# Kernel tuning notes

Measured on AMD Instinct MI355X. Metric: run time of the kernel, lower is better.

Reference implementation:

```python
import jax, jax.numpy as jnp
import numpy as np

N_ITER = 3
EPS = 1e-8


def _squash(v):
    # v: [B, 1, D]; norm over last (feature) dim
    norm = jnp.linalg.norm(v, axis=2, keepdims=True)
    scale = norm ** 2 / (1 + norm ** 2) / (norm + EPS)
    return scale * v


def setup_inputs() -> dict:
    key = jax.random.key(0)
    k1, k2 = jax.random.split(key)
    B, N, D = 64, 4096, 256
    x = jax.random.normal(k1, (B, N, D), dtype=jnp.float32)
    m = jax.random.uniform(k2, (B, N, 1), dtype=jnp.float32)
    return {"x": x, "m": m}


def reference(x, m):
    # x: [B, N, D], m: [B, N, 1]
    x = m * x
    B, N, _ = x.shape
    b = jnp.zeros((B, N, 1), dtype=x.dtype)
    s = None
    for _ in range(N_ITER):
        w = jax.nn.softmax(m * b, axis=1)            # [B, N, 1]
        sigma = jnp.sum(w * x, axis=1, keepdims=True)  # [B, 1, D]  (== bmm(w^T, x))
        s = _squash(sigma)                            # [B, 1, D]
        b_new = jnp.sum(s * x, axis=2, keepdims=True)  # [B, N, 1]
        b = b + b_new
    w = jax.nn.softmax(b, axis=1)                     # [B, N, 1]
    s = s.reshape(s.shape[0], s.shape[-1])            # [B, D]
    w = w.reshape(w.shape[0], w.shape[1])             # [B, N]
    return (w, s)
```

## Files before the change

kernel.cpp:

```cpp
#include <hip/hip_runtime.h>
#include <math.h>

#define BB 64
#define NN 4096
#define DD 256

template<bool FINAL>
__global__ __launch_bounds__(256) void fpass_kernel(
    const float* __restrict__ x, const float* __restrict__ m,
    const float* __restrict__ s_buf, float* __restrict__ b_buf,
    float* __restrict__ part_sig, float* __restrict__ part_M,
    float* __restrict__ part_Z, int P, int rowsPerWave)
{
    const int lane = threadIdx.x & 63;
    const int wib  = threadIdx.x >> 6;
    const int bpb  = P >> 2;
    const int batch = blockIdx.x / bpb;
    const int p = (blockIdx.x % bpb) * 4 + wib;
    const int n0 = p * rowsPerWave;

    const float4 s4 = reinterpret_cast<const float4*>(s_buf + batch * DD)[lane];
    const float4* __restrict__ xr =
        reinterpret_cast<const float4*>(x + ((size_t)batch * NN + n0) * DD) + lane;
    const float* __restrict__ mrow = m + (size_t)batch * NN + n0;
    float* __restrict__ brow = b_buf + (size_t)batch * NN + n0;

    float M = -INFINITY, Z = 0.f;
    float sx = 0.f, sy = 0.f, sz = 0.f, sw = 0.f;

    #pragma unroll 4
    for (int r = 0; r < rowsPerWave; ++r) {
        float4 xv = xr[(size_t)r * (DD / 4)];
        float mn = mrow[r];
        float dp = xv.x * s4.x + xv.y * s4.y + xv.z * s4.z + xv.w * s4.w;
        #pragma unroll
        for (int off = 32; off; off >>= 1) dp += __shfl_xor(dp, off, 64);
        float bn = brow[r] + mn * dp;
        if (lane == 0) brow[r] = bn;
        float l = FINAL ? bn : mn * bn;
        if (l > M) {
            float c = __expf(M - l);
            Z *= c;
            if (!FINAL) { sx *= c; sy *= c; sz *= c; sw *= c; }
            M = l;
        }
        float e = __expf(l - M);
        Z += e;
        if (!FINAL) {
            float wgt = e * mn;
            sx += wgt * xv.x; sy += wgt * xv.y; sz += wgt * xv.z; sw += wgt * xv.w;
        }
    }
    if (!FINAL) {
        reinterpret_cast<float4*>(part_sig + ((size_t)batch * P + p) * DD)[lane] =
            make_float4(sx, sy, sz, sw);
    }
    if (lane == 0) {
        part_M[batch * P + p] = M;
        part_Z[batch * P + p] = Z;
    }
}

template<bool FINAL>
__global__ __launch_bounds__(256) void reduce_kernel(
    const float* __restrict__ part_sig, const float* __restrict__ part_M,
    const float* __restrict__ part_Z, float* __restrict__ s_buf,
    float* __restrict__ s_out, float* __restrict__ MZf, int P)
{
    const int b = blockIdx.x;
    const int t = threadIdx.x;
    __shared__ float red[256];
    __shared__ float csh[128];

    float Mv = (t < P) ? part_M[b * P + t] : -INFINITY;
    red[t] = Mv;
    __syncthreads();
    for (int s = 128; s > 0; s >>= 1) {
        if (t < s) red[t] = fmaxf(red[t], red[t + s]);
        __syncthreads();
    }
    float Mg = red[0];
    __syncthreads();

    float zc = 0.f;
    if (t < P) {
        float c = expf(Mv - Mg);
        csh[t] = c;
        zc = part_Z[b * P + t] * c;
    }
    red[t] = zc;
    __syncthreads();
    for (int s = 128; s > 0; s >>= 1) {
        if (t < s) red[t] += red[t + s];
        __syncthreads();
    }
    float Zg = red[0];

    if (FINAL) {
        if (t == 0) { MZf[2 * b] = Mg; MZf[2 * b + 1] = Zg; }
        return;
    }
    __syncthreads();

    float sig = 0.f;
    for (int p = 0; p < P; ++p)
        sig += csh[p] * part_sig[((size_t)b * P + p) * DD + t];
    sig /= Zg;

    red[t] = sig * sig;
    __syncthreads();
    for (int s = 128; s > 0; s >>= 1) {
        if (t < s) red[t] += red[t + s];
        __syncthreads();
    }
    float n2 = red[0];
    float nrm = sqrtf(n2);
    float scale = n2 / (1.f + n2) / (nrm + 1e-8f);
    float sv = scale * sig;
    s_buf[b * DD + t] = sv;
    if (s_out) s_out[b * DD + t] = sv;
}

__global__ __launch_bounds__(256) void w_kernel(
    const float* __restrict__ b_buf, const float* __restrict__ MZf,
    float* __restrict__ w_out)
{
    int i = blockIdx.x * 256 + threadIdx.x;
    int b = i >> 12;
    w_out[i] = __expf(b_buf[i] - MZf[2 * b]) / MZf[2 * b + 1];
}

extern "C" void kernel_launch(void* const* d_in, const int* in_sizes, int n_in,
                              void* d_out, int out_size, void* d_ws, size_t ws_size,
                              hipStream_t stream)
{
    const float* x = (const float*)d_in[0];
    const float* m = (const float*)d_in[1];
    float* out = (float*)d_out;

    int P = 128;
    auto needBytes = [](int Pv) -> size_t {
        return (size_t)(BB * NN + BB * DD + (size_t)BB * Pv * DD + BB * Pv * 2 + 2 * BB)
               * sizeof(float);
    };
    while (P > 8 && needBytes(P) > ws_size) P >>= 1;

    float* ws       = (float*)d_ws;
    float* b_buf    = ws;
    float* s_buf    = b_buf + BB * NN;
    float* part_sig = s_buf + BB * DD;
    float* part_M   = part_sig + (size_t)BB * P * DD;
    float* part_Z   = part_M + BB * P;
    float* MZf      = part_Z + BB * P;

    hipMemsetAsync(ws, 0, (size_t)(BB * NN + BB * DD) * sizeof(float), stream);

    const int rpw = NN / P;
    const int blocksF = BB * P / 4;
    float* s_final = out + BB * NN;

    for (int it = 0; it < 3; ++it) {
        fpass_kernel<false><<<blocksF, 256, 0, stream>>>(
            x, m, s_buf, b_buf, part_sig, part_M, part_Z, P, rpw);
        reduce_kernel<false><<<BB, 256, 0, stream>>>(
            part_sig, part_M, part_Z, s_buf, (it == 2) ? s_final : nullptr, MZf, P);
    }
    fpass_kernel<true><<<blocksF, 256, 0, stream>>>(
        x, m, s_buf, b_buf, part_sig, part_M, part_Z, P, rpw);
    reduce_kernel<true><<<BB, 256, 0, stream>>>(
        part_sig, part_M, part_Z, s_buf, nullptr, MZf, P);
    w_kernel<<<BB * NN / 256, 256, 0, stream>>>(b_buf, MZf, out);
}
```

Baseline: 512.6 us.

## Unroll fpass rows by four, widen reduce kernel, vectorize softmax writer

The row loop in the fused pass now handles four rows per iteration, batching the x loads, shuffle reductions and the b/m accesses as float4, and uses a branchless online-softmax update. The partial reduction kernel moves to 1024 threads, using wave shuffles for max and sum and splitting the partial-sigma accumulation across four thread groups. The final weight kernel processes float4 per thread with a precomputed reciprocal. These aim to cut memory latency stalls and the serial reduction, at the cost of always computing two exponentials per row and requiring rowsPerWave to be a multiple of four.

```diff
diff --git a/kernel.cpp b/kernel.cpp
--- a/kernel.cpp
+++ b/kernel.cpp
@@ -28,28 +28,51 @@
     float M = -INFINITY, Z = 0.f;
     float sx = 0.f, sy = 0.f, sz = 0.f, sw = 0.f;
 
-    #pragma unroll 4
-    for (int r = 0; r < rowsPerWave; ++r) {
-        float4 xv = xr[(size_t)r * (DD / 4)];
-        float mn = mrow[r];
-        float dp = xv.x * s4.x + xv.y * s4.y + xv.z * s4.z + xv.w * s4.w;
-        #pragma unroll
-        for (int off = 32; off; off >>= 1) dp += __shfl_xor(dp, off, 64);
-        float bn = brow[r] + mn * dp;
-        if (lane == 0) brow[r] = bn;
+    auto upd = [&](float bn, float mn, const float4& xv) {
         float l = FINAL ? bn : mn * bn;
-        if (l > M) {
-            float c = __expf(M - l);
-            Z *= c;
-            if (!FINAL) { sx *= c; sy *= c; sz *= c; sw *= c; }
-            M = l;
-        }
-        float e = __expf(l - M);
-        Z += e;
+        float newM = fmaxf(M, l);
+        float c = __expf(M - newM);
+        float e = __expf(l - newM);
+        Z = Z * c + e;
         if (!FINAL) {
             float wgt = e * mn;
-            sx += wgt * xv.x; sy += wgt * xv.y; sz += wgt * xv.z; sw += wgt * xv.w;
+            sx = sx * c + wgt * xv.x;
+            sy = sy * c + wgt * xv.y;
+            sz = sz * c + wgt * xv.z;
+            sw = sw * c + wgt * xv.w;
         }
+        M = newM;
+    };
+
+    for (int r0 = 0; r0 < rowsPerWave; r0 += 4) {
+        float4 xv0 = xr[(size_t)(r0 + 0) * (DD / 4)];
+        float4 xv1 = xr[(size_t)(r0 + 1) * (DD / 4)];
+        float4 xv2 = xr[(size_t)(r0 + 2) * (DD / 4)];
+        float4 xv3 = xr[(size_t)(r0 + 3) * (DD / 4)];
+        const float4 m4 = *reinterpret_cast<const float4*>(mrow + r0);
+        const float4 b4 = *reinterpret_cast<const float4*>(brow + r0);
+
+        float dp0 = xv0.x * s4.x + xv0.y * s4.y + xv0.z * s4.z + xv0.w * s4.w;
+        float dp1 = xv1.x * s4.x + xv1.y * s4.y + xv1.z * s4.z + xv1.w * s4.w;
+        float dp2 = xv2.x * s4.x + xv2.y * s4.y + xv2.z * s4.z + xv2.w * s4.w;
+        float dp3 = xv3.x * s4.x + xv3.y * s4.y + xv3.z * s4.z + xv3.w * s4.w;
+        #pragma unroll
+        for (int off = 32; off; off >>= 1) {
+            dp0 += __shfl_xor(dp0, off, 64);
+            dp1 += __shfl_xor(dp1, off, 64);
+            dp2 += __shfl_xor(dp2, off, 64);
+            dp3 += __shfl_xor(dp3, off, 64);
+        }
+        float bn0 = b4.x + m4.x * dp0;
+        float bn1 = b4.y + m4.y * dp1;
+        float bn2 = b4.z + m4.z * dp2;
+        float bn3 = b4.w + m4.w * dp3;
+        if (lane == 0)
+            *reinterpret_cast<float4*>(brow + r0) = make_float4(bn0, bn1, bn2, bn3);
+        upd(bn0, m4.x, xv0);
+        upd(bn1, m4.y, xv1);
+        upd(bn2, m4.z, xv2);
+        upd(bn3, m4.w, xv3);
     }
     if (!FINAL) {
         reinterpret_cast<float4*>(part_sig + ((size_t)batch * P + p) * DD)[lane] =
@@ -62,63 +85,67 @@
 }
 
 template<bool FINAL>
-__global__ __launch_bounds__(256) void reduce_kernel(
+__global__ __launch_bounds__(1024) void reduce_kernel(
     const float* __restrict__ part_sig, const float* __restrict__ part_M,
     const float* __restrict__ part_Z, float* __restrict__ s_buf,
     float* __restrict__ s_out, float* __restrict__ MZf, int P)
 {
     const int b = blockIdx.x;
-    const int t = threadIdx.x;
-    __shared__ float red[256];
+    const int tid = threadIdx.x;
+    __shared__ float red[1024];
     __shared__ float csh[128];
-
-    float Mv = (t < P) ? part_M[b * P + t] : -INFINITY;
-    red[t] = Mv;
+    __shared__ float mg_sh, zg_sh;
+
+    if (tid < 64) {
+        float M0 = (tid < P) ? part_M[b * P + tid] : -INFINITY;
+        float M1 = (tid + 64 < P) ? part_M[b * P + tid + 64] : -INFINITY;
+        float Mm = fmaxf(M0, M1);
+        #pragma unroll
+        for (int off = 32; off; off >>= 1) Mm = fmaxf(Mm, __shfl_xor(Mm, off, 64));
+        float c0 = (tid < P) ? expf(M0 - Mm) : 0.f;
+        float c1 = (tid + 64 < P) ? expf(M1 - Mm) : 0.f;
+        if (tid < P) csh[tid] = c0;
+        if (tid + 64 < P) csh[tid + 64] = c1;
+        float Zs = ((tid < P) ? part_Z[b * P + tid] : 0.f) * c0
+                 + ((tid + 64 < P) ? part_Z[b * P + tid + 64] : 0.f) * c1;
+        #pragma unroll
+        for (int off = 32; off; off >>= 1) Zs += __shfl_xor(Zs, off, 64);
+        if (tid == 0) { mg_sh = Mm; zg_sh = Zs; }
+    }
+    __syncthreads();
+
+    if (FINAL) {
+        if (tid == 0) { MZf[2 * b] = mg_sh; MZf[2 * b + 1] = zg_sh; }
+        return;
+    }
+
+    const int q = tid >> 8;
+    const int d = tid & 255;
+    float sig = 0.f;
+    #pragma unroll 4
+    for (int k = q; k < P; k += 4)
+        sig += csh[k] * part_sig[((size_t)b * P + k) * DD + d];
+    red[tid] = sig;
+    __syncthreads();
+
+    if (tid < 256) {
+        sig = red[tid] + red[tid + 256] + red[tid + 512] + red[tid + 768];
+        sig /= zg_sh;
+        red[tid] = sig * sig;
+    }
     __syncthreads();
     for (int s = 128; s > 0; s >>= 1) {
-        if (t < s) red[t] = fmaxf(red[t], red[t + s]);
+        if (tid < s) red[tid] += red[tid + s];
         __syncthreads();
     }
-    float Mg = red[0];
-    __syncthreads();
-
-    float zc = 0.f;
-    if (t < P) {
-        float c = expf(Mv - Mg);
-        csh[t] = c;
-        zc = part_Z[b * P + t] * c;
-    }
-    red[t] = zc;
-    __syncthreads();
-    for (int s = 128; s > 0; s >>= 1) {
-        if (t < s) red[t] += red[t + s];
-        __syncthreads();
-    }
-    float Zg = red[0];
-
-    if (FINAL) {
-        if (t == 0) { MZf[2 * b] = Mg; MZf[2 * b + 1] = Zg; }
-        return;
-    }
-    __syncthreads();
-
-    float sig = 0.f;
-    for (int p = 0; p < P; ++p)
-        sig += csh[p] * part_sig[((size_t)b * P + p) * DD + t];
-    sig /= Zg;
-
-    red[t] = sig * sig;
-    __syncthreads();
-    for (int s = 128; s > 0; s >>= 1) {
-        if (t < s) red[t] += red[t + s];
-        __syncthreads();
-    }
-    float n2 = red[0];
-    float nrm = sqrtf(n2);
-    float scale = n2 / (1.f + n2) / (nrm + 1e-8f);
-    float sv = scale * sig;
-    s_buf[b * DD + t] = sv;
-    if (s_out) s_out[b * DD + t] = sv;
+    if (tid < 256) {
+        float n2 = red[0];
+        float nrm = sqrtf(n2);
+        float scale = n2 / (1.f + n2) / (nrm + 1e-8f);
+        float sv = scale * sig;
+        s_buf[b * DD + tid] = sv;
+        if (s_out) s_out[b * DD + tid] = sv;
+    }
 }
 
 __global__ __launch_bounds__(256) void w_kernel(
@@ -126,8 +153,16 @@
     float* __restrict__ w_out)
 {
     int i = blockIdx.x * 256 + threadIdx.x;
-    int b = i >> 12;
-    w_out[i] = __expf(b_buf[i] - MZf[2 * b]) / MZf[2 * b + 1];
+    int b = i >> 10;
+    float Mg = MZf[2 * b];
+    float iZ = 1.f / MZf[2 * b + 1];
+    float4 bv = reinterpret_cast<const float4*>(b_buf)[i];
+    float4 wv;
+    wv.x = __expf(bv.x - Mg) * iZ;
+    wv.y = __expf(bv.y - Mg) * iZ;
+    wv.z = __expf(bv.z - Mg) * iZ;
+    wv.w = __expf(bv.w - Mg) * iZ;
+    reinterpret_cast<float4*>(w_out)[i] = wv;
 }
 
 extern "C" void kernel_launch(void* const* d_in, const int* in_sizes, int n_in,
@@ -162,12 +197,12 @@
     for (int it = 0; it < 3; ++it) {
         fpass_kernel<false><<<blocksF, 256, 0, stream>>>(
             x, m, s_buf, b_buf, part_sig, part_M, part_Z, P, rpw);
-        reduce_kernel<false><<<BB, 256, 0, stream>>>(
+        reduce_kernel<false><<<BB, 1024, 0, stream>>>(
             part_sig, part_M, part_Z, s_buf, (it == 2) ? s_final : nullptr, MZf, P);
     }
     fpass_kernel<true><<<blocksF, 256, 0, stream>>>(
         x, m, s_buf, b_buf, part_sig, part_M, part_Z, P, rpw);
-    reduce_kernel<true><<<BB, 256, 0, stream>>>(
+    reduce_kernel<true><<<BB, 1024, 0, stream>>>(
         part_sig, part_M, part_Z, s_buf, nullptr, MZf, P);
-    w_kernel<<<BB * NN / 256, 256, 0, stream>>>(b_buf, MZf, out);
-}
+    w_kernel<<<BB * NN / 1024, 256, 0, stream>>>(b_buf, MZf, out);
+}
```

New measurement: 514.3 us. Within noise of the previous version (+0.3%).
